# Optimization experiments

Measured on AMD Instinct MI355X. Metric: run time of the kernel, lower is better.

The kernel has to match this reference:

```python
import jax, jax.numpy as jnp
import numpy as np

B, S, D = 2, 2048, 1024
H = 16
HD = D // H  # 64


def setup_inputs() -> dict:
    key = jax.random.key(0)
    ks = jax.random.split(key, 6)
    scale = 1.0 / np.sqrt(D)
    return {
        "x": jax.random.normal(ks[0], (B, S, D), dtype=jnp.float32),
        "W_q": jax.random.normal(ks[1], (D, D), dtype=jnp.float32) * scale,
        "W_k": jax.random.normal(ks[2], (D, D), dtype=jnp.float32) * scale,
        "W_v": jax.random.normal(ks[3], (D, D), dtype=jnp.float32) * scale,
        "W_o": jax.random.normal(ks[4], (D, D), dtype=jnp.float32) * scale,
        "b_o": jax.random.normal(ks[5], (D,), dtype=jnp.float32) * 0.01,
    }


def reference(x, W_q, W_k, W_v, W_o, b_o):
    # Projections (torch Linear applies x @ W.T; weights here stored as [out, in])
    q = jnp.einsum("bsd,ed->bse", x, W_q).reshape(B, S, H, HD)
    k = jnp.einsum("bsd,ed->bse", x, W_k).reshape(B, S, H, HD)
    v = jnp.einsum("bsd,ed->bse", x, W_v).reshape(B, S, H, HD)
    # scores: [B, H, S, S]
    scores = jnp.einsum("bqhd,bkhd->bhqk", q, k) / jnp.sqrt(jnp.float32(HD))
    attn = jax.nn.softmax(scores, axis=-1)
    # dropout is identity in eval mode
    out = jnp.einsum("bhqk,bkhd->bqhd", attn, v).reshape(B, S, D)
    return jnp.einsum("bsd,ed->bse", out, W_o) + b_o
```

## Files before the change

### kernel.cpp

```cpp
#include <hip/hip_runtime.h>
#include <hip/hip_bf16.h>

typedef __hip_bfloat16 bf16_t;
typedef __bf16 bf16x8 __attribute__((ext_vector_type(8)));
typedef __bf16 bf16x4 __attribute__((ext_vector_type(4)));
typedef short  s16x4  __attribute__((ext_vector_type(4)));
typedef float  f32x4  __attribute__((ext_vector_type(4)));

#define MFMA(a, b, c) __builtin_amdgcn_mfma_f32_16x16x32_bf16((a), (b), (c), 0, 0, 0)

__device__ __forceinline__ f32x4 mfma16(bf16x4 a, bf16x4 b, f32x4 c) {
#if __has_builtin(__builtin_amdgcn_mfma_f32_16x16x16_bf16)
  return __builtin_amdgcn_mfma_f32_16x16x16_bf16(a, b, c, 0, 0, 0);
#else
  return __builtin_amdgcn_mfma_f32_16x16x16bf16_1k(
      __builtin_bit_cast(s16x4, a), __builtin_bit_cast(s16x4, b), c, 0, 0, 0);
#endif
}

__device__ __forceinline__ bf16x8 ldg8(const bf16_t* p) {
  return *reinterpret_cast<const bf16x8*>(p);
}
__device__ __forceinline__ bf16x4 ldg4(const bf16_t* p) {
  return *reinterpret_cast<const bf16x4*>(p);
}
__device__ __forceinline__ void st8(bf16_t* p, bf16x8 v) {
  *reinterpret_cast<bf16x8*>(p) = v;
}
__device__ __forceinline__ void store_out(bf16_t* p, float v) { *p = __float2bfloat16(v); }
__device__ __forceinline__ void store_out(float* p, float v)  { *p = v; }

__device__ __forceinline__ void async16(const bf16_t* g, bf16_t* l) {
  __builtin_amdgcn_global_load_lds(
      (const __attribute__((address_space(1))) void*)g,
      (__attribute__((address_space(3))) void*)l, 16, 0, 0);
}

__global__ __launch_bounds__(256) void cvt_kernel(
    const float* __restrict__ x,  const float* __restrict__ Wq,
    const float* __restrict__ Wk, const float* __restrict__ Wv,
    const float* __restrict__ Wo,
    bf16_t* __restrict__ xb,  bf16_t* __restrict__ Wqb,
    bf16_t* __restrict__ Wkb, bf16_t* __restrict__ Wvb,
    bf16_t* __restrict__ Wob) {
  const int bid = blockIdx.x;
  const float* src; bf16_t* dst; size_t base;
  float scl = 1.0f;
  if (bid < 2048)      { src = x;  dst = xb;  base = (size_t)bid * 2048; }
  else if (bid < 2560) { src = Wq; dst = Wqb; base = (size_t)(bid - 2048) * 2048;
                         scl = 0.180336878f; }
  else if (bid < 3072) { src = Wk; dst = Wkb; base = (size_t)(bid - 2560) * 2048; }
  else if (bid < 3584) { src = Wv; dst = Wvb; base = (size_t)(bid - 3072) * 2048; }
  else                 { src = Wo; dst = Wob; base = (size_t)(bid - 3584) * 2048; }
  const size_t i0 = base + (size_t)threadIdx.x * 8;
  const float4 f0 = *reinterpret_cast<const float4*>(src + i0);
  const float4 f1 = *reinterpret_cast<const float4*>(src + i0 + 4);
  bf16x8 v;
  v[0] = (__bf16)(f0.x * scl); v[1] = (__bf16)(f0.y * scl);
  v[2] = (__bf16)(f0.z * scl); v[3] = (__bf16)(f0.w * scl);
  v[4] = (__bf16)(f1.x * scl); v[5] = (__bf16)(f1.y * scl);
  v[6] = (__bf16)(f1.z * scl); v[7] = (__bf16)(f1.w * scl);
  st8(dst + i0, v);
}

#define GK 1024

template <typename OutT, bool BIAS>
__device__ __forceinline__ void gemm_tile(
    const bf16_t* __restrict__ A, const bf16_t* __restrict__ B,
    OutT* __restrict__ C, const float* __restrict__ bias,
    int bm, int bn, int ldc, bf16_t* As, bf16_t* Bs) {
  const int tid  = threadIdx.x;
  const int lane = tid & 63;
  const int wave = tid >> 6;
  const int wm   = (wave & 1) << 6;
  const int wn   = (wave >> 1) << 6;
  const int lr   = lane & 15;
  const int lq   = lane >> 4;

  const int srow = tid >> 3;
  const int sx   = ((tid & 7) ^ (srow & 7)) << 3;

  const bf16_t* Ag = A + (size_t)(bm + srow) * GK + sx;
  const bf16_t* Bg = B + (size_t)(bn + srow) * GK + sx;
  bf16_t* Asw = As + wave * 512;
  bf16_t* Bsw = Bs + wave * 512;

  f32x4 acc[4][4];
#pragma unroll
  for (int i = 0; i < 4; ++i)
#pragma unroll
    for (int j = 0; j < 4; ++j) acc[i][j] = (f32x4){0.f, 0.f, 0.f, 0.f};

  for (int k0 = 0; k0 < GK; k0 += 64) {
    __syncthreads();
#pragma unroll
    for (int g = 0; g < 4; ++g) {
      async16(Ag + k0 + (size_t)(g * 32) * GK, Asw + g * 2048);
      async16(Bg + k0 + (size_t)(g * 32) * GK, Bsw + g * 2048);
    }
    __syncthreads();
#pragma unroll
    for (int ks = 0; ks < 2; ++ks) {
      bf16x8 af[4], bf[4];
      const int chs = ((ks * 4 + lq) ^ (lr & 7)) << 3;
#pragma unroll
      for (int i = 0; i < 4; ++i) {
        af[i] = ldg8(&As[(wm + i * 16 + lr) * 64 + chs]);
        bf[i] = ldg8(&Bs[(wn + i * 16 + lr) * 64 + chs]);
      }
#pragma unroll
      for (int mi = 0; mi < 4; ++mi)
#pragma unroll
        for (int ni = 0; ni < 4; ++ni)
          acc[mi][ni] = MFMA(af[mi], bf[ni], acc[mi][ni]);
    }
  }

#pragma unroll
  for (int ni = 0; ni < 4; ++ni) {
    const int col = bn + wn + ni * 16 + lr;
    float bv = 0.f;
    if (BIAS) bv = bias[col];
#pragma unroll
    for (int mi = 0; mi < 4; ++mi) {
#pragma unroll
      for (int r = 0; r < 4; ++r) {
        const int row = bm + wm + mi * 16 + lq * 4 + r;
        store_out(&C[(size_t)row * ldc + col], acc[mi][ni][r] + bv);
      }
    }
  }
}

__global__ __launch_bounds__(256) void qkv_kernel(
    const bf16_t* __restrict__ x, const bf16_t* __restrict__ Wq,
    const bf16_t* __restrict__ Wk, const bf16_t* __restrict__ Wv,
    bf16_t* __restrict__ Q, bf16_t* __restrict__ Kp, bf16_t* __restrict__ Vt) {
  __shared__ alignas(16) bf16_t As[128 * 64];
  __shared__ alignas(16) bf16_t Bs[128 * 64];
  const int bid = blockIdx.x;
  const int z   = blockIdx.y;
  const int mt  = (bid & 31) * 128;
  const int nt  = (bid >> 5) * 128;
  if (z == 0) {
    gemm_tile<bf16_t, false>(x, Wq, Q, nullptr, mt, nt, 1024, As, Bs);
  } else if (z == 1) {
    gemm_tile<bf16_t, false>(x, Wk, Kp, nullptr, mt, nt, 1024, As, Bs);
  } else {
    gemm_tile<bf16_t, false>(Wv, x, Vt, nullptr, nt, mt, 4096, As, Bs);
  }
}

__global__ __launch_bounds__(256) void out_proj_kernel(
    const bf16_t* __restrict__ Ao, const bf16_t* __restrict__ Wo,
    const float* __restrict__ bias, float* __restrict__ out) {
  __shared__ alignas(16) bf16_t As[128 * 64];
  __shared__ alignas(16) bf16_t Bs[128 * 64];
  const int bid = blockIdx.x;
  gemm_tile<float, true>(Ao, Wo, out, bias, (bid & 31) * 128, (bid >> 5) * 128, 1024, As, Bs);
}

#define VPAD 68

__global__ __launch_bounds__(256) void attn_kernel(
    const bf16_t* __restrict__ Q, const bf16_t* __restrict__ Kp,
    const bf16_t* __restrict__ Vt, bf16_t* __restrict__ Ao) {
  __shared__ alignas(16) char smem_raw[4 * 64 * 17 * 4];
  bf16_t* Ks = (bf16_t*)smem_raw;
  bf16_t* Vs = (bf16_t*)(smem_raw + 8192);
  float*  Osc = (float*)smem_raw;

  const int tid  = threadIdx.x;
  const int lane = tid & 63;
  const int wave = tid >> 6;
  const int lr   = lane & 15;
  const int lq   = lane >> 4;
  const int bh   = blockIdx.x;
  const int qt   = blockIdx.y;
  const int b    = bh >> 4;
  const int h    = bh & 15;
  const size_t tok0 = (size_t)b * 2048;
  const int col0 = h * 64;
  const int qblk = qt * 128 + wave * 32;

  bf16x8 qf[2][2];
#pragma unroll
  for (int nt = 0; nt < 2; ++nt) {
    const size_t qrow = tok0 + qblk + nt * 16 + lr;
#pragma unroll
    for (int c = 0; c < 2; ++c)
      qf[nt][c] = ldg8(&Q[qrow * 1024 + col0 + c * 32 + lq * 8]);
  }

  f32x4 o[2][4];
#pragma unroll
  for (int nt = 0; nt < 2; ++nt)
#pragma unroll
    for (int i = 0; i < 4; ++i) o[nt][i] = (f32x4){0.f, 0.f, 0.f, 0.f};
  float lsum[2] = {0.f, 0.f};

  const int srow = tid >> 3;
  const int sxk  = ((tid & 7) ^ (srow & 7)) << 3;
  const int sxv  = (tid & 7) << 3;
  bf16_t* Ksw = Ks + wave * 512;

  const int koff0 = lr * 64 + ((lq ^ (lr & 7)) << 3);
  const int koff1 = lr * 64 + (((lq + 4) ^ (lr & 7)) << 3);
  const int voff  = lr * VPAD + lq * 4;

  for (int kv0 = 0; kv0 < 2048; kv0 += 64) {
    const bf16_t* Kg = Kp + (tok0 + kv0) * 1024 + col0;
    const bf16_t* Vg = Vt + (size_t)col0 * 4096 + tok0 + kv0;
    const bf16x8 v0 = ldg8(Vg + (size_t)srow * 4096 + sxv);
    const bf16x8 v1 = ldg8(Vg + (size_t)(srow + 32) * 4096 + sxv);
    __syncthreads();
    async16(Kg + (size_t)srow * 1024 + sxk, Ksw);
    async16(Kg + (size_t)(srow + 32) * 1024 + sxk, Ksw + 2048);
    st8(&Vs[srow * VPAD + sxv], v0);
    st8(&Vs[(srow + 32) * VPAD + sxv], v1);
    __syncthreads();

#pragma unroll
    for (int c = 0; c < 4; ++c) {
      const bf16x8 kf0 = ldg8(&Ks[c * 1024 + koff0]);
      const bf16x8 kf1 = ldg8(&Ks[c * 1024 + koff1]);
      bf16x4 pb[2];
#pragma unroll
      for (int nt = 0; nt < 2; ++nt) {
        f32x4 sT = {0.f, 0.f, 0.f, 0.f};
        sT = MFMA(kf0, qf[nt][0], sT);
        sT = MFMA(kf1, qf[nt][1], sT);
        const float p0 = exp2f(sT.x);
        const float p1 = exp2f(sT.y);
        const float p2 = exp2f(sT.z);
        const float p3 = exp2f(sT.w);
        pb[nt][0] = (__bf16)p0; pb[nt][1] = (__bf16)p1;
        pb[nt][2] = (__bf16)p2; pb[nt][3] = (__bf16)p3;
        lsum[nt] += (p0 + p1) + (p2 + p3);
      }
#pragma unroll
      for (int ht = 0; ht < 4; ++ht) {
        const bf16x4 vf = ldg4(&Vs[ht * 16 * VPAD + voff + c * 16]);
        o[0][ht] = mfma16(vf, pb[0], o[0][ht]);
        o[1][ht] = mfma16(vf, pb[1], o[1][ht]);
      }
    }
  }

  __syncthreads();

  float* Ow = &Osc[wave * 64 * 17];
#pragma unroll
  for (int nt = 0; nt < 2; ++nt) {
    float ls = lsum[nt];
    ls += __shfl_xor(ls, 16);
    ls += __shfl_xor(ls, 32);
    const float invl = 1.f / ls;

#pragma unroll
    for (int ht = 0; ht < 4; ++ht)
#pragma unroll
      for (int r = 0; r < 4; ++r)
        Ow[(ht * 16 + lq * 4 + r) * 17 + lr] = o[nt][ht][r] * invl;

    const int qq = lane >> 2;
    const int hc = (lane & 3) * 16;
    bf16x8 w0, w1;
#pragma unroll
    for (int i = 0; i < 8; ++i) {
      w0[i] = (__bf16)Ow[(hc + i) * 17 + qq];
      w1[i] = (__bf16)Ow[(hc + 8 + i) * 17 + qq];
    }
    bf16_t* dst = Ao + (tok0 + qblk + nt * 16 + qq) * 1024 + col0 + hc;
    st8(dst, w0);
    st8(dst + 8, w1);
  }
}

extern "C" void kernel_launch(void* const* d_in, const int* in_sizes, int n_in,
                              void* d_out, int out_size, void* d_ws, size_t ws_size,
                              hipStream_t stream) {
  const float* x  = (const float*)d_in[0];
  const float* Wq = (const float*)d_in[1];
  const float* Wk = (const float*)d_in[2];
  const float* Wv = (const float*)d_in[3];
  const float* Wo = (const float*)d_in[4];
  const float* bo = (const float*)d_in[5];
  float* out = (float*)d_out;

  const size_t NTOK = 4096, DMODEL = 1024, WSZ = DMODEL * DMODEL;
  bf16_t* xb  = (bf16_t*)d_ws;
  bf16_t* Wqb = xb + NTOK * DMODEL;
  bf16_t* Wkb = Wqb + WSZ;
  bf16_t* Wvb = Wkb + WSZ;
  bf16_t* Wob = Wvb + WSZ;
  bf16_t* Q   = Wob + WSZ;
  bf16_t* Kp  = Q  + NTOK * DMODEL;
  bf16_t* Vt  = Kp + NTOK * DMODEL;
  bf16_t* Ao  = Vt + NTOK * DMODEL;

  cvt_kernel<<<dim3(4096), 256, 0, stream>>>(x, Wq, Wk, Wv, Wo, xb, Wqb, Wkb, Wvb, Wob);
  qkv_kernel<<<dim3(256, 3), 256, 0, stream>>>(xb, Wqb, Wkb, Wvb, Q, Kp, Vt);
  attn_kernel<<<dim3(32, 16), 256, 0, stream>>>(Q, Kp, Vt, Ao);
  out_proj_kernel<<<dim3(256, 1), 256, 0, stream>>>(Ao, Wob, bo, out);
}
```

Measured before the change: 209.2 us.

## Split attention KV tiles across waves and reduce partial outputs via LDS atomics

The attention kernel changes from giving each wave 32 query rows over the whole KV tile to having all four waves share a 64-query block, each wave taking a 16-key slice of every 64-key tile. Partial O accumulators and row sums are combined across waves with LDS float atomicAdds before normalization and the bf16 store. The grid doubles to 32x32 blocks and launch bounds request 3 blocks per SM. This cuts per-wave LDS reads of K/V fragments and raises block count for occupancy, at the cost of an atomic reduction epilogue and twice as many global K/V tile loads in total.

```diff
diff --git a/kernel.cpp b/kernel.cpp
--- a/kernel.cpp
+++ b/kernel.cpp
@@ -162,14 +162,16 @@
 }
 
 #define VPAD 68
-
-__global__ __launch_bounds__(256) void attn_kernel(
+#define OPAD 66
+
+__global__ __launch_bounds__(256, 3) void attn_kernel(
     const bf16_t* __restrict__ Q, const bf16_t* __restrict__ Kp,
     const bf16_t* __restrict__ Vt, bf16_t* __restrict__ Ao) {
-  __shared__ alignas(16) char smem_raw[4 * 64 * 17 * 4];
-  bf16_t* Ks = (bf16_t*)smem_raw;
-  bf16_t* Vs = (bf16_t*)(smem_raw + 8192);
+  __shared__ alignas(16) char smem_raw[64 * OPAD * 4];
+  bf16_t* Ks  = (bf16_t*)smem_raw;
+  bf16_t* Vs  = (bf16_t*)(smem_raw + 8192);
   float*  Osc = (float*)smem_raw;
+  __shared__ float Llds[64];
 
   const int tid  = threadIdx.x;
   const int lane = tid & 63;
@@ -182,32 +184,34 @@
   const int h    = bh & 15;
   const size_t tok0 = (size_t)b * 2048;
   const int col0 = h * 64;
-  const int qblk = qt * 128 + wave * 32;
-
-  bf16x8 qf[2][2];
-#pragma unroll
-  for (int nt = 0; nt < 2; ++nt) {
-    const size_t qrow = tok0 + qblk + nt * 16 + lr;
+
+  if (tid < 64) Llds[tid] = 0.f;
+
+  bf16x8 qf[4][2];
+#pragma unroll
+  for (int nt = 0; nt < 4; ++nt) {
+    const size_t qrow = tok0 + qt * 64 + nt * 16 + lr;
 #pragma unroll
     for (int c = 0; c < 2; ++c)
       qf[nt][c] = ldg8(&Q[qrow * 1024 + col0 + c * 32 + lq * 8]);
   }
 
-  f32x4 o[2][4];
-#pragma unroll
-  for (int nt = 0; nt < 2; ++nt)
-#pragma unroll
-    for (int i = 0; i < 4; ++i) o[nt][i] = (f32x4){0.f, 0.f, 0.f, 0.f};
-  float lsum[2] = {0.f, 0.f};
+  f32x4 o[4][4];
+#pragma unroll
+  for (int i = 0; i < 4; ++i)
+#pragma unroll
+    for (int j = 0; j < 4; ++j) o[i][j] = (f32x4){0.f, 0.f, 0.f, 0.f};
+  float lsum[4] = {0.f, 0.f, 0.f, 0.f};
 
   const int srow = tid >> 3;
   const int sxk  = ((tid & 7) ^ (srow & 7)) << 3;
   const int sxv  = (tid & 7) << 3;
   bf16_t* Ksw = Ks + wave * 512;
 
-  const int koff0 = lr * 64 + ((lq ^ (lr & 7)) << 3);
-  const int koff1 = lr * 64 + (((lq + 4) ^ (lr & 7)) << 3);
-  const int voff  = lr * VPAD + lq * 4;
+  const int kRowOff = (wave * 16 + lr) * 64;
+  const int kOff0   = kRowOff + ((lq ^ (lr & 7)) << 3);
+  const int kOff1   = kRowOff + (((lq + 4) ^ (lr & 7)) << 3);
+  const int vOff    = lr * VPAD + wave * 16 + lq * 4;
 
   for (int kv0 = 0; kv0 < 2048; kv0 += 64) {
     const bf16_t* Kg = Kp + (tok0 + kv0) * 1024 + col0;
@@ -221,61 +225,61 @@
     st8(&Vs[(srow + 32) * VPAD + sxv], v1);
     __syncthreads();
 
-#pragma unroll
-    for (int c = 0; c < 4; ++c) {
-      const bf16x8 kf0 = ldg8(&Ks[c * 1024 + koff0]);
-      const bf16x8 kf1 = ldg8(&Ks[c * 1024 + koff1]);
-      bf16x4 pb[2];
-#pragma unroll
-      for (int nt = 0; nt < 2; ++nt) {
-        f32x4 sT = {0.f, 0.f, 0.f, 0.f};
-        sT = MFMA(kf0, qf[nt][0], sT);
-        sT = MFMA(kf1, qf[nt][1], sT);
-        const float p0 = exp2f(sT.x);
-        const float p1 = exp2f(sT.y);
-        const float p2 = exp2f(sT.z);
-        const float p3 = exp2f(sT.w);
-        pb[nt][0] = (__bf16)p0; pb[nt][1] = (__bf16)p1;
-        pb[nt][2] = (__bf16)p2; pb[nt][3] = (__bf16)p3;
-        lsum[nt] += (p0 + p1) + (p2 + p3);
-      }
-#pragma unroll
-      for (int ht = 0; ht < 4; ++ht) {
-        const bf16x4 vf = ldg4(&Vs[ht * 16 * VPAD + voff + c * 16]);
-        o[0][ht] = mfma16(vf, pb[0], o[0][ht]);
-        o[1][ht] = mfma16(vf, pb[1], o[1][ht]);
-      }
+    const bf16x8 kf0 = ldg8(&Ks[kOff0]);
+    const bf16x8 kf1 = ldg8(&Ks[kOff1]);
+    bf16x4 vf[4];
+#pragma unroll
+    for (int ht = 0; ht < 4; ++ht) vf[ht] = ldg4(&Vs[(ht * 16 + lr) * VPAD] + (vOff - lr * VPAD));
+
+#pragma unroll
+    for (int nt = 0; nt < 4; ++nt) {
+      f32x4 sT = {0.f, 0.f, 0.f, 0.f};
+      sT = MFMA(kf0, qf[nt][0], sT);
+      sT = MFMA(kf1, qf[nt][1], sT);
+      const float p0 = exp2f(sT.x);
+      const float p1 = exp2f(sT.y);
+      const float p2 = exp2f(sT.z);
+      const float p3 = exp2f(sT.w);
+      bf16x4 pb;
+      pb[0] = (__bf16)p0; pb[1] = (__bf16)p1;
+      pb[2] = (__bf16)p2; pb[3] = (__bf16)p3;
+      lsum[nt] += (p0 + p1) + (p2 + p3);
+#pragma unroll
+      for (int ht = 0; ht < 4; ++ht)
+        o[nt][ht] = mfma16(vf[ht], pb, o[nt][ht]);
     }
   }
 
   __syncthreads();
-
-  float* Ow = &Osc[wave * 64 * 17];
-#pragma unroll
-  for (int nt = 0; nt < 2; ++nt) {
+  for (int i = tid; i < 64 * OPAD; i += 256) Osc[i] = 0.f;
+  __syncthreads();
+
+#pragma unroll
+  for (int nt = 0; nt < 4; ++nt) {
+#pragma unroll
+    for (int ht = 0; ht < 4; ++ht)
+#pragma unroll
+      for (int r = 0; r < 4; ++r)
+        atomicAdd(&Osc[(ht * 16 + lq * 4 + r) * OPAD + nt * 16 + lr], o[nt][ht][r]);
     float ls = lsum[nt];
     ls += __shfl_xor(ls, 16);
     ls += __shfl_xor(ls, 32);
-    const float invl = 1.f / ls;
-
-#pragma unroll
-    for (int ht = 0; ht < 4; ++ht)
-#pragma unroll
-      for (int r = 0; r < 4; ++r)
-        Ow[(ht * 16 + lq * 4 + r) * 17 + lr] = o[nt][ht][r] * invl;
-
-    const int qq = lane >> 2;
-    const int hc = (lane & 3) * 16;
-    bf16x8 w0, w1;
-#pragma unroll
-    for (int i = 0; i < 8; ++i) {
-      w0[i] = (__bf16)Ow[(hc + i) * 17 + qq];
-      w1[i] = (__bf16)Ow[(hc + 8 + i) * 17 + qq];
-    }
-    bf16_t* dst = Ao + (tok0 + qblk + nt * 16 + qq) * 1024 + col0 + hc;
-    st8(dst, w0);
-    st8(dst + 8, w1);
-  }
+    if (lq == 0) atomicAdd(&Llds[nt * 16 + lr], ls);
+  }
+  __syncthreads();
+
+  const int q  = tid >> 2;
+  const int hs = (tid & 3) * 16;
+  const float invl = 1.f / Llds[q];
+  bf16x8 w0, w1;
+#pragma unroll
+  for (int i = 0; i < 8; ++i) {
+    w0[i] = (__bf16)(Osc[(hs + i) * OPAD + q] * invl);
+    w1[i] = (__bf16)(Osc[(hs + 8 + i) * OPAD + q] * invl);
+  }
+  bf16_t* dst = Ao + (tok0 + qt * 64 + q) * 1024 + col0 + hs;
+  st8(dst, w0);
+  st8(dst + 8, w1);
 }
 
 extern "C" void kernel_launch(void* const* d_in, const int* in_sizes, int n_in,
@@ -302,6 +306,6 @@
 
   cvt_kernel<<<dim3(4096), 256, 0, stream>>>(x, Wq, Wk, Wv, Wo, xb, Wqb, Wkb, Wvb, Wob);
   qkv_kernel<<<dim3(256, 3), 256, 0, stream>>>(xb, Wqb, Wkb, Wvb, Q, Kp, Vt);
-  attn_kernel<<<dim3(32, 16), 256, 0, stream>>>(Q, Kp, Vt, Ao);
+  attn_kernel<<<dim3(32, 32), 256, 0, stream>>>(Q, Kp, Vt, Ao);
   out_proj_kernel<<<dim3(256, 1), 256, 0, stream>>>(Ao, Wob, bo, out);
 }
```

Result: slower. 284.5 us (+36.0%).
